# Kernel tuning notes

Hardware: AMD Instinct MI355X
Metric: run time of the kernel (lower is better)

Reference implementation:

```python
import jax, jax.numpy as jnp
import numpy as np

HIDDEN = 2048
NUM_HEADS = 16
HEAD_DIM = HIDDEN // NUM_HEADS
SCALE = 1.0 / np.sqrt(HEAD_DIM).astype(np.float32)
BATCH, SEQ = 2, 2048


def setup_inputs() -> dict:
    key = jax.random.key(0)
    ks = jax.random.split(key, 9)
    std = 0.02
    inp = {
        'hidden_states': jax.random.normal(ks[0], (BATCH, SEQ, HIDDEN), jnp.float32),
        'attention_mask': jnp.zeros((BATCH, 1, 1, SEQ), jnp.float32),
        'Wq': jax.random.normal(ks[1], (HIDDEN, HIDDEN), jnp.float32) * std,
        'bq': jnp.zeros((HIDDEN,), jnp.float32),
        'Wk': jax.random.normal(ks[2], (HIDDEN, HIDDEN), jnp.float32) * std,
        'bk': jnp.zeros((HIDDEN,), jnp.float32),
        'Wv': jax.random.normal(ks[3], (HIDDEN, HIDDEN), jnp.float32) * std,
        'bv': jnp.zeros((HIDDEN,), jnp.float32),
        'Wo': jax.random.normal(ks[4], (HIDDEN, HIDDEN), jnp.float32) * std,
        'bo': jnp.zeros((HIDDEN,), jnp.float32),
    }
    return inp


def _split_heads(x):
    b, s, _ = x.shape
    return x.reshape(b, s, NUM_HEADS, HEAD_DIM).transpose(0, 2, 1, 3)  # [b,h,s,d]


def reference(hidden_states, attention_mask, Wq, bq, Wk, bk, Wv, bv, Wo, bo):
    # Linear layers (torch convention: y = x @ W.T + b)
    q = _split_heads(hidden_states @ Wq.T + bq)
    k = _split_heads(hidden_states @ Wk.T + bk)
    v = _split_heads(hidden_states @ Wv.T + bv)
    scores = jnp.einsum('bhqd,bhkd->bhqk', q, k) * SCALE
    scores = scores + attention_mask
    weights = jax.nn.softmax(scores, axis=-1)  # dropout is identity in eval
    ctx = jnp.einsum('bhqk,bhkd->bhqd', weights, v)
    b, h, s, d = ctx.shape
    ctx = ctx.transpose(0, 2, 1, 3).reshape(b, s, HIDDEN)
    return ctx @ Wo.T + bo
```

## Files before the change

kernel.cpp:

```cpp
#include <hip/hip_runtime.h>

typedef __bf16 bf16_t;
typedef bf16_t bf16x8 __attribute__((ext_vector_type(8)));
typedef float f32x4 __attribute__((ext_vector_type(4)));

#define HIDDEN 2048
#define SEQ 2048
#define BATCH 2
#define NHEADS 16
#define HDIM 128
#define MTOT (BATCH*SEQ)
#define SCALE 0.088388347648318447f
#define C1EXP2 0.12753102158508967f
#define LOG2E  1.4426950408889634f

__device__ __forceinline__ float dev_exp2(float x) { return __builtin_amdgcn_exp2f(x); }

typedef __attribute__((address_space(1))) const void gvoid_t;
typedef __attribute__((address_space(3))) void svoid_t;
__device__ __forceinline__ void async_copy16(const bf16_t* g, bf16_t* l) {
  __builtin_amdgcn_global_load_lds((gvoid_t*)g, (svoid_t*)l, 16, 0, 0);
}

__global__ void cvt_all(const float* __restrict__ x,  const float* __restrict__ wq,
                        const float* __restrict__ wk, const float* __restrict__ wv,
                        const float* __restrict__ wo,
                        bf16_t* __restrict__ xb, bf16_t* __restrict__ wqkb,
                        bf16_t* __restrict__ wvb, bf16_t* __restrict__ wob) {
  const size_t HH = (size_t)HIDDEN * HIDDEN;
  const float* src; bf16_t* dst;
  switch (blockIdx.y) {
    case 0:  src = x;        dst = xb;        break;
    case 1:  src = x + HH;   dst = xb + HH;   break;
    case 2:  src = wq;       dst = wqkb;      break;
    case 3:  src = wk;       dst = wqkb + HH; break;
    case 4:  src = wv;       dst = wvb;       break;
    default: src = wo;       dst = wob;       break;
  }
  int i = blockIdx.x * 256 + threadIdx.x;
  float4 v = reinterpret_cast<const float4*>(src)[i];
  union { bf16_t h[4]; uint2 u; } t;
  t.h[0] = (bf16_t)v.x; t.h[1] = (bf16_t)v.y; t.h[2] = (bf16_t)v.z; t.h[3] = (bf16_t)v.w;
  reinterpret_cast<uint2*>(dst)[i] = t.u;
}

__global__ void pack_bias2(const float* __restrict__ a, const float* __restrict__ b2,
                           float* __restrict__ out) {
  int i = blockIdx.x * 256 + threadIdx.x;
  out[i] = (i < HIDDEN) ? a[i] : b2[i - HIDDEN];
}

template<bool OUT_BF16, bool ROW_BIAS>
__global__ __launch_bounds__(256, 3)
void gemm_bt(const bf16_t* __restrict__ A, const bf16_t* __restrict__ Bt,
             const float* __restrict__ bias, void* __restrict__ Yv,
             int M, int N, int K, int ldY) {
  __shared__ __align__(16) bf16_t As[128 * 32];
  __shared__ __align__(16) bf16_t Bs[128 * 32];
  const int tid  = threadIdx.x;
  const int lane = tid & 63;
  const int wv   = tid >> 6;
  const int wr   = wv >> 1, wc = wv & 1;
  const int lr   = lane & 15, quad = lane >> 4;
  const int n0   = blockIdx.x * 128;
  const int m0   = blockIdx.y * 128;

  f32x4 acc[4][4] = {};

  const int srow = wv * 16 + (lane >> 2);
  const int scol = (lane & 3) * 8;
  const bf16_t* gA = A  + (size_t)(m0 + srow) * K + scol;
  const bf16_t* gB = Bt + (size_t)(n0 + srow) * K + scol;
  bf16_t* lA = &As[wv * 16 * 32];
  bf16_t* lB = &Bs[wv * 16 * 32];
  const size_t step64 = (size_t)64 * K;

  for (int kt = 0; kt < K; kt += 32) {
    __syncthreads();
    async_copy16(gA,          lA);
    async_copy16(gA + step64, lA + 64 * 32);
    async_copy16(gB,          lB);
    async_copy16(gB + step64, lB + 64 * 32);
    gA += 32; gB += 32;
    __syncthreads();
    bf16x8 af[4], bfr[4];
#pragma unroll
    for (int mi = 0; mi < 4; ++mi)
      af[mi] = *(const bf16x8*)&As[(wr * 64 + mi * 16 + lr) * 32 + quad * 8];
#pragma unroll
    for (int ni = 0; ni < 4; ++ni)
      bfr[ni] = *(const bf16x8*)&Bs[(wc * 64 + ni * 16 + lr) * 32 + quad * 8];
#pragma unroll
    for (int mi = 0; mi < 4; ++mi)
#pragma unroll
      for (int ni = 0; ni < 4; ++ni)
        acc[mi][ni] = __builtin_amdgcn_mfma_f32_16x16x32_bf16(af[mi], bfr[ni], acc[mi][ni], 0, 0, 0);
  }

  float bcol[4];
  if (!ROW_BIAS) {
#pragma unroll
    for (int ni = 0; ni < 4; ++ni) bcol[ni] = bias[n0 + wc * 64 + ni * 16 + lr];
  }
#pragma unroll
  for (int mi = 0; mi < 4; ++mi) {
#pragma unroll
    for (int r = 0; r < 4; ++r) {
      int row = m0 + wr * 64 + mi * 16 + quad * 4 + r;
      float brow = ROW_BIAS ? bias[row] : 0.0f;
      size_t base = (size_t)row * ldY + n0 + wc * 64;
#pragma unroll
      for (int ni = 0; ni < 4; ++ni) {
        float y = acc[mi][ni][r] + (ROW_BIAS ? brow : bcol[ni]);
        int col = ni * 16 + lr;
        if (OUT_BF16) ((bf16_t*)Yv)[base + col] = (bf16_t)y;
        else          ((float*)Yv)[base + col]  = y;
      }
    }
  }
}

#define BQ 64
#define BKV 64
#define LDQK 4096

__global__ __launch_bounds__(128, 2)
void attn_kernel(const bf16_t* __restrict__ QK, const bf16_t* __restrict__ Vt,
                 const float* __restrict__ mask, bf16_t* __restrict__ O) {
  __shared__ __align__(16) bf16_t Ks[BKV * 128];
  __shared__ __align__(16) bf16_t Vs[HDIM * BKV];
  __shared__ __align__(16) bf16_t Ps[BQ * BKV];

  const int tid  = threadIdx.x;
  const int lane = tid & 63;
  const int wv   = tid >> 6;
  const int lr   = lane & 15, quad = lane >> 4;
  const int q0   = blockIdx.x * BQ;
  const int bh   = blockIdx.y;
  const int b    = bh >> 4, h = bh & 15;

  const bf16_t* Qg = QK + (size_t)(b * SEQ + q0) * LDQK + h * HDIM;
  const bf16_t* Kg = QK + (size_t)(b * SEQ) * LDQK + HIDDEN + h * HDIM;
  const bf16_t* Vg = Vt + (size_t)(h * HDIM) * MTOT + b * SEQ;
  const float*  mb = mask + b * SEQ;

  bf16x8 qf[2][4];
#pragma unroll
  for (int mi = 0; mi < 2; ++mi)
#pragma unroll
    for (int dk = 0; dk < 4; ++dk)
      qf[mi][dk] = *(const bf16x8*)(Qg + (size_t)(wv * 32 + mi * 16 + lr) * LDQK + dk * 32 + quad * 8);

  const int kcs = lane & 15;
  const int vcs = lane & 7;
  const bf16_t* kgp[8]; const bf16_t* vgp[8];
  int lKo[8], lVo[8];
#pragma unroll
  for (int i = 0; i < 8; ++i) {
    int kr = wv * 32 + i * 4 + (lane >> 4);
    kgp[i] = Kg + (size_t)kr * LDQK + ((kcs ^ (kr & 15)) * 8);
    lKo[i] = (wv * 32 + i * 4) * 128;
    int vr = wv * 64 + i * 8 + (lane >> 3);
    vgp[i] = Vg + (size_t)vr * MTOT + ((vcs ^ (vr & 7)) * 8);
    lVo[i] = (wv * 64 + i * 8) * 64;
  }

  float l_st[2][4] = {};
  f32x4 oacc[2][8] = {};

  for (int kt = 0; kt < SEQ; kt += BKV) {
    __syncthreads();
#pragma unroll
    for (int i = 0; i < 8; ++i) async_copy16(kgp[i] + (size_t)kt * LDQK, &Ks[lKo[i]]);
#pragma unroll
    for (int i = 0; i < 8; ++i) async_copy16(vgp[i] + kt, &Vs[lVo[i]]);
    __syncthreads();

    float mk[4];
#pragma unroll
    for (int ni = 0; ni < 4; ++ni) mk[ni] = mb[kt + ni * 16 + lr] * LOG2E;

    f32x4 sacc[2][4] = {};
#pragma unroll
    for (int dk = 0; dk < 4; ++dk) {
      bf16x8 kf[4];
#pragma unroll
      for (int ni = 0; ni < 4; ++ni)
        kf[ni] = *(const bf16x8*)&Ks[(ni * 16 + lr) * 128 + (((dk * 4 + quad) ^ lr) * 8)];
#pragma unroll
      for (int mi = 0; mi < 2; ++mi)
#pragma unroll
        for (int ni = 0; ni < 4; ++ni)
          sacc[mi][ni] = __builtin_amdgcn_mfma_f32_16x16x32_bf16(qf[mi][dk], kf[ni], sacc[mi][ni], 0, 0, 0);
    }

#pragma unroll
    for (int mi = 0; mi < 2; ++mi) {
#pragma unroll
      for (int r = 0; r < 4; ++r) {
        float p0 = dev_exp2(fmaf(sacc[mi][0][r], C1EXP2, mk[0]));
        float p1 = dev_exp2(fmaf(sacc[mi][1][r], C1EXP2, mk[1]));
        float p2 = dev_exp2(fmaf(sacc[mi][2][r], C1EXP2, mk[2]));
        float p3 = dev_exp2(fmaf(sacc[mi][3][r], C1EXP2, mk[3]));
        int pr = wv * 32 + mi * 16 + quad * 4 + r;
        int key = pr & 7;
        Ps[pr * BKV + (((0 + (lr >> 3)) ^ key) * 8) + (lr & 7)] = (bf16_t)p0;
        Ps[pr * BKV + (((2 + (lr >> 3)) ^ key) * 8) + (lr & 7)] = (bf16_t)p1;
        Ps[pr * BKV + (((4 + (lr >> 3)) ^ key) * 8) + (lr & 7)] = (bf16_t)p2;
        Ps[pr * BKV + (((6 + (lr >> 3)) ^ key) * 8) + (lr & 7)] = (bf16_t)p3;
        l_st[mi][r] += (p0 + p1) + (p2 + p3);
      }
    }

#pragma unroll
    for (int ki = 0; ki < 2; ++ki) {
      bf16x8 pf[2];
#pragma unroll
      for (int mi = 0; mi < 2; ++mi)
        pf[mi] = *(const bf16x8*)&Ps[(wv * 32 + mi * 16 + lr) * BKV + (((ki * 4 + quad) ^ (lr & 7)) * 8)];
#pragma unroll
      for (int di = 0; di < 8; ++di) {
        bf16x8 vf = *(const bf16x8*)&Vs[(di * 16 + lr) * BKV + (((ki * 4 + quad) ^ (lr & 7)) * 8)];
#pragma unroll
        for (int mi = 0; mi < 2; ++mi)
          oacc[mi][di] = __builtin_amdgcn_mfma_f32_16x16x32_bf16(pf[mi], vf, oacc[mi][di], 0, 0, 0);
      }
    }
  }

  bf16_t* Ob = O + (size_t)(b * SEQ + q0) * HIDDEN + h * HDIM;
#pragma unroll
  for (int mi = 0; mi < 2; ++mi) {
#pragma unroll
    for (int r = 0; r < 4; ++r) {
      float s = l_st[mi][r];
      s += __shfl_xor(s, 1);
      s += __shfl_xor(s, 2);
      s += __shfl_xor(s, 4);
      s += __shfl_xor(s, 8);
      float inv = 1.0f / s;
      size_t rowoff = (size_t)(wv * 32 + mi * 16 + quad * 4 + r) * HIDDEN;
#pragma unroll
      for (int di = 0; di < 8; ++di)
        Ob[rowoff + di * 16 + lr] = (bf16_t)(oacc[mi][di][r] * inv);
    }
  }
}

extern "C" void kernel_launch(void* const* d_in, const int* in_sizes, int n_in,
                              void* d_out, int out_size, void* d_ws, size_t ws_size,
                              hipStream_t stream) {
  const float* x   = (const float*)d_in[0];
  const float* msk = (const float*)d_in[1];
  const float* Wq  = (const float*)d_in[2];
  const float* bq  = (const float*)d_in[3];
  const float* Wk  = (const float*)d_in[4];
  const float* bk  = (const float*)d_in[5];
  const float* Wv  = (const float*)d_in[6];
  const float* bv  = (const float*)d_in[7];
  const float* Wo  = (const float*)d_in[8];
  const float* bo  = (const float*)d_in[9];
  float* out = (float*)d_out;

  bf16_t* Xb   = (bf16_t*)d_ws;
  bf16_t* Wqkb = Xb   + (size_t)MTOT * HIDDEN;
  bf16_t* Wvb  = Wqkb + (size_t)2 * HIDDEN * HIDDEN;
  bf16_t* Wob  = Wvb  + (size_t)HIDDEN * HIDDEN;
  bf16_t* QKo  = Wob  + (size_t)HIDDEN * HIDDEN;
  bf16_t* Vto  = QKo  + (size_t)MTOT * 2 * HIDDEN;
  float*  bqk  = (float*)(Vto + (size_t)HIDDEN * MTOT);
  bf16_t* Cb   = Xb;

  cvt_all<<<dim3(HIDDEN * HIDDEN / 4 / 256, 6), 256, 0, stream>>>(
      x, Wq, Wk, Wv, Wo, Xb, Wqkb, Wvb, Wob);
  pack_bias2<<<2 * HIDDEN / 256, 256, 0, stream>>>(bq, bk, bqk);

  gemm_bt<true, false><<<dim3(32, 32), 256, 0, stream>>>(Xb, Wqkb, bqk, QKo,
                                                         MTOT, 2 * HIDDEN, HIDDEN, 2 * HIDDEN);
  gemm_bt<true, true><<<dim3(32, 16), 256, 0, stream>>>(Wvb, Xb, bv, Vto,
                                                        HIDDEN, MTOT, HIDDEN, MTOT);
  attn_kernel<<<dim3(SEQ / BQ, BATCH * NHEADS), 128, 0, stream>>>(QKo, Vto, msk, Cb);
  gemm_bt<false, false><<<dim3(16, 32), 256, 0, stream>>>(Cb, Wob, bo, out,
                                                          MTOT, HIDDEN, HIDDEN, HIDDEN);
}
```

Baseline: 423.8 us.

## Double-buffer K tiles, widen attention blocks to 128 queries, cache mask in LDS

The attention kernel now runs 4 waves over 128 query rows per block, which halves the number of K/V tile loads per query. K tiles are double-buffered: the next tile is prefetched while the current one is used, and the V load is overlapped with the QK^T and softmax phase. Explicit waitcnt and barrier control replaces __syncthreads. The mask is preloaded once into LDS, pre-scaled by log2(e). The cost is more LDS per block (extra K buffer plus an 8KB mask), which may reduce occupancy, and the hand-counted vmcnt values must match the number of copies in flight.

```diff
diff --git a/kernel.cpp b/kernel.cpp
--- a/kernel.cpp
+++ b/kernel.cpp
@@ -120,16 +120,17 @@
   }
 }
 
-#define BQ 64
+#define BQ 128
 #define BKV 64
 #define LDQK 4096
 
-__global__ __launch_bounds__(128, 2)
+__global__ __launch_bounds__(256, 2)
 void attn_kernel(const bf16_t* __restrict__ QK, const bf16_t* __restrict__ Vt,
                  const float* __restrict__ mask, bf16_t* __restrict__ O) {
-  __shared__ __align__(16) bf16_t Ks[BKV * 128];
+  __shared__ __align__(16) bf16_t Ks[2][BKV * 128];
   __shared__ __align__(16) bf16_t Vs[HDIM * BKV];
   __shared__ __align__(16) bf16_t Ps[BQ * BKV];
+  __shared__ __align__(16) float  Msk[SEQ];
 
   const int tid  = threadIdx.x;
   const int lane = tid & 63;
@@ -151,34 +152,59 @@
     for (int dk = 0; dk < 4; ++dk)
       qf[mi][dk] = *(const bf16x8*)(Qg + (size_t)(wv * 32 + mi * 16 + lr) * LDQK + dk * 32 + quad * 8);
 
+  for (int i = tid; i < SEQ / 4; i += 256) {
+    float4 mv = reinterpret_cast<const float4*>(mb)[i];
+    Msk[i * 4 + 0] = mv.x * LOG2E;
+    Msk[i * 4 + 1] = mv.y * LOG2E;
+    Msk[i * 4 + 2] = mv.z * LOG2E;
+    Msk[i * 4 + 3] = mv.w * LOG2E;
+  }
+
   const int kcs = lane & 15;
   const int vcs = lane & 7;
-  const bf16_t* kgp[8]; const bf16_t* vgp[8];
-  int lKo[8], lVo[8];
-#pragma unroll
-  for (int i = 0; i < 8; ++i) {
-    int kr = wv * 32 + i * 4 + (lane >> 4);
+  const bf16_t* kgp[4]; const bf16_t* vgp[4];
+  int lKo[4], lVo[4];
+#pragma unroll
+  for (int i = 0; i < 4; ++i) {
+    int kr = wv * 16 + i * 4 + (lane >> 4);
     kgp[i] = Kg + (size_t)kr * LDQK + ((kcs ^ (kr & 15)) * 8);
-    lKo[i] = (wv * 32 + i * 4) * 128;
-    int vr = wv * 64 + i * 8 + (lane >> 3);
+    lKo[i] = (wv * 16 + i * 4) * 128;
+    int vr = wv * 32 + i * 8 + (lane >> 3);
     vgp[i] = Vg + (size_t)vr * MTOT + ((vcs ^ (vr & 7)) * 8);
-    lVo[i] = (wv * 64 + i * 8) * 64;
-  }
+    lVo[i] = (wv * 32 + i * 8) * 64;
+  }
+
+  asm volatile("s_waitcnt vmcnt(0)" ::: "memory");
+#pragma unroll
+  for (int i = 0; i < 4; ++i) async_copy16(kgp[i], &Ks[0][lKo[i]]);
+  asm volatile("s_waitcnt lgkmcnt(0)" ::: "memory");
+  __builtin_amdgcn_s_barrier();
 
   float l_st[2][4] = {};
   f32x4 oacc[2][8] = {};
 
   for (int kt = 0; kt < SEQ; kt += BKV) {
-    __syncthreads();
-#pragma unroll
-    for (int i = 0; i < 8; ++i) async_copy16(kgp[i] + (size_t)kt * LDQK, &Ks[lKo[i]]);
-#pragma unroll
-    for (int i = 0; i < 8; ++i) async_copy16(vgp[i] + kt, &Vs[lVo[i]]);
-    __syncthreads();
+    const int cur = (kt >> 6) & 1;
+    const bf16_t* Kc = &Ks[cur][0];
+
+    asm volatile("s_waitcnt lgkmcnt(0)" ::: "memory");
+    __builtin_amdgcn_s_barrier();
+#pragma unroll
+    for (int i = 0; i < 4; ++i) async_copy16(vgp[i] + kt, &Vs[lVo[i]]);
+    if (kt + BKV < SEQ) {
+#pragma unroll
+      for (int i = 0; i < 4; ++i)
+        async_copy16(kgp[i] + (size_t)(kt + BKV) * LDQK, &Ks[cur ^ 1][lKo[i]]);
+      asm volatile("s_waitcnt vmcnt(8)" ::: "memory");
+    } else {
+      asm volatile("s_waitcnt vmcnt(4)" ::: "memory");
+    }
+    __builtin_amdgcn_s_barrier();
+    __builtin_amdgcn_sched_barrier(0);
 
     float mk[4];
 #pragma unroll
-    for (int ni = 0; ni < 4; ++ni) mk[ni] = mb[kt + ni * 16 + lr] * LOG2E;
+    for (int ni = 0; ni < 4; ++ni) mk[ni] = Msk[kt + ni * 16 + lr];
 
     f32x4 sacc[2][4] = {};
 #pragma unroll
@@ -186,7 +212,7 @@
       bf16x8 kf[4];
 #pragma unroll
       for (int ni = 0; ni < 4; ++ni)
-        kf[ni] = *(const bf16x8*)&Ks[(ni * 16 + lr) * 128 + (((dk * 4 + quad) ^ lr) * 8)];
+        kf[ni] = *(const bf16x8*)&Kc[(ni * 16 + lr) * 128 + (((dk * 4 + quad) ^ lr) * 8)];
 #pragma unroll
       for (int mi = 0; mi < 2; ++mi)
 #pragma unroll
@@ -211,6 +237,14 @@
         l_st[mi][r] += (p0 + p1) + (p2 + p3);
       }
     }
+
+    if (kt + BKV < SEQ) {
+      asm volatile("s_waitcnt vmcnt(4)" ::: "memory");
+    } else {
+      asm volatile("s_waitcnt vmcnt(0)" ::: "memory");
+    }
+    __builtin_amdgcn_s_barrier();
+    __builtin_amdgcn_sched_barrier(0);
 
 #pragma unroll
     for (int ki = 0; ki < 2; ++ki) {
@@ -279,7 +313,7 @@
                                                          MTOT, 2 * HIDDEN, HIDDEN, 2 * HIDDEN);
   gemm_bt<true, true><<<dim3(32, 16), 256, 0, stream>>>(Wvb, Xb, bv, Vto,
                                                         HIDDEN, MTOT, HIDDEN, MTOT);
-  attn_kernel<<<dim3(SEQ / BQ, BATCH * NHEADS), 128, 0, stream>>>(QKo, Vto, msk, Cb);
+  attn_kernel<<<dim3(SEQ / BQ, BATCH * NHEADS), 256, 0, stream>>>(QKo, Vto, msk, Cb);
   gemm_bt<false, false><<<dim3(16, 32), 256, 0, stream>>>(Cb, Wob, bo, out,
                                                           MTOT, HIDDEN, HIDDEN, HIDDEN);
 }
```

Measured after the change: 421.5 us. No clear change (-0.5%).
